# Optimization experiments

Measured on AMD Instinct MI355X. Metric: run time of the kernel, lower is better.

Reference implementation:

```python
import jax, jax.numpy as jnp
import numpy as np

ITERATIONS = 2   # init kwarg 'iterations'
EPS = 1e-7


def squash(s):
    # squash along last axis (dims_out), matching squash(..., axis=-2) on [..., dims, 1]
    sq_norm = jnp.sum(s * s, axis=-1, keepdims=True)
    return (sq_norm / (1.0 + sq_norm)) * s / jnp.sqrt(sq_norm + EPS)


def setup_inputs() -> dict:
    key = jax.random.key(0)
    kx, kw = jax.random.split(key)
    B, C_IN, D_IN = 64, 2048, 8    # batch, input capsules, input capsule dims
    K, D_OUT = 32, 16              # output capsules (caps), output dims (dims)
    x = jax.random.normal(kx, (B, C_IN, D_IN), dtype=jnp.float32)
    # W ~ Normal(0, 0.1) as in add_weight initializer; stored [K, C_IN, D_OUT, D_IN]
    W = jax.random.normal(kw, (K, C_IN, D_OUT, D_IN), dtype=jnp.float32) * 0.1
    return {"x": x, "W": W}


def reference(x, W):
    # predictions u[b,k,c,i] = sum_j W[k,c,i,j] * x[b,c,j]
    u = jnp.einsum('kcij,bcj->bkci', W, x)          # [B, K, C, D_OUT]
    B, K, C, D = u.shape
    logits = jnp.zeros((B, K, C), dtype=u.dtype)
    v = jnp.zeros((B, K, D), dtype=u.dtype)         # initial_outputs = 0
    for _ in range(ITERATIONS):
        # agreement[b,k,c] = <u[b,k,c,:], v[b,k,:]>  (predictions^T @ outputs)
        agreement = jnp.einsum('bkci,bki->bkc', u, v)
        logits = logits + agreement
        # softmax over output capsules (original axis=3 == caps_out dim)
        cc = jax.nn.softmax(logits, axis=1)          # [B, K, C]
        s = jnp.einsum('bkc,bkci->bki', cc, u)       # centroids: sum over caps_in
        v = squash(s)                                # [B, K, D]
    return v
```

## Files before the change

### kernel.cpp

```cpp
#include <hip/hip_runtime.h>

#define Bn 64
#define Cn 2048
#define Kn 32
#define In 16
#define EPSf 1e-7f

#define NOUT (Bn * Kn * In)
#define KJ   (Cn * 8)
#define KS1  64
#define KS2  32

typedef short bf8v __attribute__((ext_vector_type(8)));
typedef float f4v  __attribute__((ext_vector_type(4)));

union U16B { uint4 u; bf8v v; unsigned short h[8]; };

__device__ __forceinline__ unsigned short f2bf(float f) {
    unsigned u = __float_as_uint(f);
    u += 0x7FFF + ((u >> 16) & 1);
    return (unsigned short)(u >> 16);
}
__device__ __forceinline__ unsigned cvtpk(float lo, float hi) {
    unsigned r;
    asm("v_cvt_pk_bf16_f32 %0, %1, %2" : "=v"(r) : "v"(lo), "v"(hi));
    return r;
}
__device__ __forceinline__ float bflo(unsigned u) { return __uint_as_float(u << 16); }
__device__ __forceinline__ float bfhi(unsigned u) { return __uint_as_float(u & 0xffff0000u); }

__global__ __launch_bounds__(256) void kPrepX(const float* __restrict__ x,
                                              unsigned short* __restrict__ xb,
                                              unsigned short* __restrict__ xT2)
{
    const int g = blockIdx.x * 256 + threadIdx.x;
    const float4* s = (const float4*)(x + (size_t)g * 8);
    float4 a = s[0], b4 = s[1];
    U16B o;
    o.h[0] = f2bf(a.x);  o.h[1] = f2bf(a.y);  o.h[2] = f2bf(a.z);  o.h[3] = f2bf(a.w);
    o.h[4] = f2bf(b4.x); o.h[5] = f2bf(b4.y); o.h[6] = f2bf(b4.z); o.h[7] = f2bf(b4.w);
    ((uint4*)xb)[g] = o.u;
    const int b = g >> 11, c = g & 2047;
    *(uint2*)(xT2 + ((size_t)(c * 2 + 0) * 64 + b) * 4) = make_uint2(o.u.x, o.u.y);
    *(uint2*)(xT2 + ((size_t)(c * 2 + 1) * 64 + b) * 4) = make_uint2(o.u.z, o.u.w);
}

__global__ __launch_bounds__(256) void kGemm1(const unsigned short* __restrict__ xb,
                                              const float* __restrict__ W,
                                              float* __restrict__ part1)
{
    const int nstrip = blockIdx.x & 7;
    const int ksplit = blockIdx.x >> 3;
    const int ks0    = ksplit * 8;
    const int lane   = threadIdx.x & 63;
    const int m0     = (threadIdx.x >> 6) * 16;
    const int i      = lane & 15;
    const int cq     = lane >> 4;

    f4v acc[4] = {};
    const unsigned short* arow = xb + (size_t)(m0 + (lane & 15)) * KJ + cq * 8;

    for (int s = 0; s < 8; ++s) {
        const int ks = ks0 + s;
        U16B af;
        af.u = *(const uint4*)(arow + (size_t)ks * 32);
        const int c = ks * 4 + cq;
        #pragma unroll
        for (int t = 0; t < 4; ++t) {
            const int ko = nstrip * 4 + t;
            const float* wp = W + (((size_t)ko * Cn + c) * 16 + i) * 8;
            const float4 w0 = *(const float4*)wp;
            const float4 w1 = *(const float4*)(wp + 4);
            U16B bf;
            bf.u.x = cvtpk(w0.x, w0.y); bf.u.y = cvtpk(w0.z, w0.w);
            bf.u.z = cvtpk(w1.x, w1.y); bf.u.w = cvtpk(w1.z, w1.w);
            acc[t] = __builtin_amdgcn_mfma_f32_16x16x32_bf16(af.v, bf.v, acc[t], 0, 0, 0);
        }
    }

    float* pb = part1 + (size_t)ksplit * NOUT;
    const int col = lane & 15, rbase = (lane >> 4) * 4;
    #pragma unroll
    for (int t = 0; t < 4; ++t) {
        const int n = (nstrip * 4 + t) * 16 + col;
        #pragma unroll
        for (int r = 0; r < 4; ++r)
            pb[(size_t)(m0 + rbase + r) * 512 + n] = acc[t][r];
    }
}

__global__ __launch_bounds__(256) void kSq1(const float* __restrict__ part1,
                                            unsigned short* __restrict__ v1f)
{
    const int t = blockIdx.x * 256 + threadIdx.x;
    float s = 0.f;
    #pragma unroll 8
    for (int g = 0; g < KS1; ++g) s += part1[(size_t)g * NOUT + t];
    s *= (1.0f / 32.0f);
    float sq = s * s;
    sq += __shfl_xor(sq, 1);
    sq += __shfl_xor(sq, 2);
    sq += __shfl_xor(sq, 4);
    sq += __shfl_xor(sq, 8);
    const float f = (sq / (1.0f + sq)) * rsqrtf(sq + EPSf);
    const float v = s * f;
    const int b = t >> 9, k = (t >> 4) & 31, i = t & 15;
    const int pos = ((k * 4 + (b >> 4)) * 32 + (i >> 3) * 16 + (b & 15)) * 8 + (i & 7);
    v1f[pos] = f2bf(v);
}

__global__ __launch_bounds__(256) void kAgr(const float* __restrict__ W,
                                            const unsigned short* __restrict__ v1f,
                                            const unsigned short* __restrict__ xT2,
                                            float* __restrict__ agr)
{
    const int ko   = blockIdx.x & 31;
    const int cg   = blockIdx.x >> 5;
    const int lane = threadIdx.x & 63;
    const int w    = threadIdx.x >> 6;

    U16B bfr[4];
    #pragma unroll
    for (int nt = 0; nt < 4; ++nt) {
        if (lane < 32)
            bfr[nt].u = *(const uint4*)(v1f + ((size_t)(ko * 4 + nt) * 32 + lane) * 8);
        else
            bfr[nt].u = make_uint4(0, 0, 0, 0);
    }

    for (int mt = w; mt < 32; mt += 4) {
        const int cjb = cg * 512 + mt * 16;
        U16B afr;
        if (lane < 32) {
            const int cj = cjb + (lane & 15);
            const int c = cj >> 3, j = cj & 7;
            const int ib = (lane >> 4) * 8;
            const float* wp = W + (((size_t)ko * Cn + c) * 16 + ib) * 8 + j;
            afr.u.x = cvtpk(wp[0],  wp[8]);
            afr.u.y = cvtpk(wp[16], wp[24]);
            afr.u.z = cvtpk(wp[32], wp[40]);
            afr.u.w = cvtpk(wp[48], wp[56]);
        } else afr.u = make_uint4(0, 0, 0, 0);

        const int xrow = (cjb >> 2) + (lane >> 4);
        #pragma unroll
        for (int nt = 0; nt < 4; ++nt) {
            f4v acc = {0.f, 0.f, 0.f, 0.f};
            acc = __builtin_amdgcn_mfma_f32_16x16x32_bf16(afr.v, bfr[nt].v, acc, 0, 0, 0);
            const int b = nt * 16 + (lane & 15);
            const uint2 xq = *(const uint2*)(xT2 + ((size_t)xrow * 64 + b) * 4);
            float p = acc[0] * bflo(xq.x) + acc[1] * bfhi(xq.x)
                    + acc[2] * bflo(xq.y) + acc[3] * bfhi(xq.y);
            p += __shfl_xor(p, 16);
            if (!(lane & 16)) {
                const int c = (cjb >> 3) + (lane >> 5);
                agr[((size_t)ko * Cn + c) * 64 + b] = p;
            }
        }
    }
}

__global__ __launch_bounds__(256) void kSmax(float* __restrict__ agr)
{
    const int t = blockIdx.x * 256 + threadIdx.x;
    float* base = agr + (size_t)(t >> 6) * 64 + (t & 63);
    float a[32];
    float mx = -1e30f;
    #pragma unroll
    for (int k = 0; k < 32; ++k) { a[k] = base[(size_t)k * (Cn * 64)]; mx = fmaxf(mx, a[k]); }
    float sum = 0.f;
    #pragma unroll
    for (int k = 0; k < 32; ++k) { a[k] = __expf(a[k] - mx); sum += a[k]; }
    const float r = 1.0f / sum;
    #pragma unroll
    for (int k = 0; k < 32; ++k) base[(size_t)k * (Cn * 64)] = a[k] * r;
}

__global__ __launch_bounds__(256) void kGemm2(const unsigned short* __restrict__ xb,
                                              const float* __restrict__ W,
                                              const float* __restrict__ cc,
                                              float* __restrict__ part2)
{
    const int ko    = blockIdx.x & 31;
    const int split = blockIdx.x >> 5;
    const int ks0   = split * 16;
    const int lane  = threadIdx.x & 63;
    const int m0    = (threadIdx.x >> 6) * 16;
    const int i     = lane & 15;
    const int cq    = lane >> 4;
    const int bg    = m0 + (lane & 15);

    f4v acc = {0.f, 0.f, 0.f, 0.f};
    const unsigned short* arow = xb + (size_t)bg * KJ + cq * 8;
    const float* ccp = cc + ((size_t)ko * Cn + ks0 * 4 + cq) * 64 + bg;

    for (int s = 0; s < 16; ++s) {
        const int ks = ks0 + s;
        const int c  = ks * 4 + cq;
        const uint4 au = *(const uint4*)(arow + (size_t)ks * 32);
        const float cv = ccp[s * 256];
        U16B af;
        af.u.x = cvtpk(bflo(au.x) * cv, bfhi(au.x) * cv);
        af.u.y = cvtpk(bflo(au.y) * cv, bfhi(au.y) * cv);
        af.u.z = cvtpk(bflo(au.z) * cv, bfhi(au.z) * cv);
        af.u.w = cvtpk(bflo(au.w) * cv, bfhi(au.w) * cv);
        const float* wp = W + (((size_t)ko * Cn + c) * 16 + i) * 8;
        const float4 w0 = *(const float4*)wp;
        const float4 w1 = *(const float4*)(wp + 4);
        U16B bf;
        bf.u.x = cvtpk(w0.x, w0.y); bf.u.y = cvtpk(w0.z, w0.w);
        bf.u.z = cvtpk(w1.x, w1.y); bf.u.w = cvtpk(w1.z, w1.w);
        acc = __builtin_amdgcn_mfma_f32_16x16x32_bf16(af.v, bf.v, acc, 0, 0, 0);
    }

    float* pb = part2 + (size_t)split * NOUT;
    const int col = lane & 15, rbase = (lane >> 4) * 4;
    #pragma unroll
    for (int r = 0; r < 4; ++r)
        pb[(size_t)(m0 + rbase + r) * 512 + ko * 16 + col] = acc[r];
}

__global__ __launch_bounds__(256) void kSq2(const float* __restrict__ part2,
                                            float* __restrict__ out)
{
    const int t = blockIdx.x * 256 + threadIdx.x;
    const size_t o = (size_t)t * 4;
    float4 s = make_float4(0.f, 0.f, 0.f, 0.f);
    #pragma unroll 8
    for (int g = 0; g < KS2; ++g) {
        const float4 p = *(const float4*)(part2 + (size_t)g * NOUT + o);
        s.x += p.x; s.y += p.y; s.z += p.z; s.w += p.w;
    }
    float sq = (s.x * s.x + s.y * s.y) + (s.z * s.z + s.w * s.w);
    sq += __shfl_xor(sq, 1);
    sq += __shfl_xor(sq, 2);
    const float f = (sq / (1.0f + sq)) * rsqrtf(sq + EPSf);
    *(float4*)(out + o) = make_float4(s.x * f, s.y * f, s.z * f, s.w * f);
}

extern "C" void kernel_launch(void* const* d_in, const int* in_sizes, int n_in,
                              void* d_out, int out_size, void* d_ws, size_t ws_size,
                              hipStream_t stream)
{
    const float* x = (const float*)d_in[0];
    const float* W = (const float*)d_in[1];
    float* out = (float*)d_out;

    float* wsf = (float*)d_ws;
    float*          agr   = wsf;
    float*          part1 = wsf;
    unsigned short* xb    = (unsigned short*)(wsf + 4194304);
    unsigned short* xT2   = (unsigned short*)(wsf + 4194304 + 524288);
    float*          part2 = wsf + 4194304 + 524288;
    unsigned short* v1f   = (unsigned short*)(wsf + 4194304 + 524288 + 1048576);

    kPrepX<<<512,  256, 0, stream>>>(x, xb, xT2);
    kGemm1<<<512,  256, 0, stream>>>(xb, W, part1);
    kSq1  <<<128,  256, 0, stream>>>(part1, v1f);
    kAgr  <<<1024, 256, 0, stream>>>(W, v1f, xT2, agr);
    kSmax <<<512,  256, 0, stream>>>(agr);
    kGemm2<<<1024, 256, 0, stream>>>(xb, W, agr, part2);
    kSq2  <<<32,   256, 0, stream>>>(part2, out);
}
```

Before: 136.6 us.

## Fuse all routing stages into one cooperative persistent kernel with grid syncs

Merges the seven separate kernels into a single cooperative kernel of 512 blocks. Stages are separated by grid-wide barriers, and the code falls back to per-phase launches if the cooperative launch fails. Each stage is re-partitioned to fit the fixed 512-block grid: agreement and the second GEMM do twice the work per block, the split-K of the second GEMM drops from 32 to 16, and the reductions use shared memory. The goal is to remove launch gaps between kernels. In exchange it adds grid-sync cost, fewer blocks for the larger phases, and register pressure from the combined kernel.

Result: slower. 505.6 us (+270.2%).

```diff
diff --git a/kernel.cpp b/kernel.cpp
--- a/kernel.cpp
+++ b/kernel.cpp
@@ -1,15 +1,15 @@
 #include <hip/hip_runtime.h>
-
-#define Bn 64
+#include <hip/hip_cooperative_groups.h>
+
+namespace cg = cooperative_groups;
+
 #define Cn 2048
-#define Kn 32
-#define In 16
 #define EPSf 1e-7f
 
-#define NOUT (Bn * Kn * In)
-#define KJ   (Cn * 8)
+#define NOUT 32768
+#define KJ   16384
 #define KS1  64
-#define KS2  32
+#define KS2  16
 
 typedef short bf8v __attribute__((ext_vector_type(8)));
 typedef float f4v  __attribute__((ext_vector_type(4)));
@@ -29,213 +29,232 @@
 __device__ __forceinline__ float bflo(unsigned u) { return __uint_as_float(u << 16); }
 __device__ __forceinline__ float bfhi(unsigned u) { return __uint_as_float(u & 0xffff0000u); }
 
-__global__ __launch_bounds__(256) void kPrepX(const float* __restrict__ x,
-                                              unsigned short* __restrict__ xb,
-                                              unsigned short* __restrict__ xT2)
+__global__ __launch_bounds__(256, 4) void kFused(const float* __restrict__ x,
+                                                 const float* __restrict__ W,
+                                                 float* __restrict__ out,
+                                                 float* __restrict__ wsf,
+                                                 int phase)
 {
-    const int g = blockIdx.x * 256 + threadIdx.x;
-    const float4* s = (const float4*)(x + (size_t)g * 8);
-    float4 a = s[0], b4 = s[1];
-    U16B o;
-    o.h[0] = f2bf(a.x);  o.h[1] = f2bf(a.y);  o.h[2] = f2bf(a.z);  o.h[3] = f2bf(a.w);
-    o.h[4] = f2bf(b4.x); o.h[5] = f2bf(b4.y); o.h[6] = f2bf(b4.z); o.h[7] = f2bf(b4.w);
-    ((uint4*)xb)[g] = o.u;
-    const int b = g >> 11, c = g & 2047;
-    *(uint2*)(xT2 + ((size_t)(c * 2 + 0) * 64 + b) * 4) = make_uint2(o.u.x, o.u.y);
-    *(uint2*)(xT2 + ((size_t)(c * 2 + 1) * 64 + b) * 4) = make_uint2(o.u.z, o.u.w);
-}
-
-__global__ __launch_bounds__(256) void kGemm1(const unsigned short* __restrict__ xb,
-                                              const float* __restrict__ W,
-                                              float* __restrict__ part1)
-{
-    const int nstrip = blockIdx.x & 7;
-    const int ksplit = blockIdx.x >> 3;
-    const int ks0    = ksplit * 8;
-    const int lane   = threadIdx.x & 63;
-    const int m0     = (threadIdx.x >> 6) * 16;
-    const int i      = lane & 15;
-    const int cq     = lane >> 4;
-
-    f4v acc[4] = {};
-    const unsigned short* arow = xb + (size_t)(m0 + (lane & 15)) * KJ + cq * 8;
-
-    for (int s = 0; s < 8; ++s) {
-        const int ks = ks0 + s;
-        U16B af;
-        af.u = *(const uint4*)(arow + (size_t)ks * 32);
-        const int c = ks * 4 + cq;
+    float*          agr   = wsf;
+    float*          part1 = wsf;
+    unsigned short* xb    = (unsigned short*)(wsf + 4194304);
+    unsigned short* xT2   = (unsigned short*)(wsf + 4718592);
+    float*          part2 = wsf + 4718592;
+    unsigned short* v1f   = (unsigned short*)(wsf + 5242880);
+
+    cg::grid_group grid = cg::this_grid();
+    const int  bid  = blockIdx.x;
+    const int  tid  = threadIdx.x;
+    const int  lane = tid & 63;
+    const bool all  = (phase < 0);
+
+    __shared__ float  shA[4][65];
+    __shared__ float4 shB[256];
+
+    if (all || phase == 0) {
+        const int g = bid * 256 + tid;
+        const float4* s = (const float4*)(x + (size_t)g * 8);
+        float4 a = s[0], b4 = s[1];
+        U16B o;
+        o.h[0] = f2bf(a.x);  o.h[1] = f2bf(a.y);  o.h[2] = f2bf(a.z);  o.h[3] = f2bf(a.w);
+        o.h[4] = f2bf(b4.x); o.h[5] = f2bf(b4.y); o.h[6] = f2bf(b4.z); o.h[7] = f2bf(b4.w);
+        ((uint4*)xb)[g] = o.u;
+        const int b = g >> 11, c = g & 2047;
+        *(uint2*)(xT2 + ((size_t)(c * 2 + 0) * 64 + b) * 4) = make_uint2(o.u.x, o.u.y);
+        *(uint2*)(xT2 + ((size_t)(c * 2 + 1) * 64 + b) * 4) = make_uint2(o.u.z, o.u.w);
+    }
+    if (all) grid.sync();
+
+    if (all || phase == 1) {
+        const int nstrip = bid & 7;
+        const int ksplit = bid >> 3;
+        const int ks0    = ksplit * 8;
+        const int m0     = (tid >> 6) * 16;
+        const int i      = lane & 15;
+        const int cq     = lane >> 4;
+
+        f4v acc[4] = {};
+        const unsigned short* arow = xb + (size_t)(m0 + i) * KJ + cq * 8;
+
+        for (int s = 0; s < 8; ++s) {
+            const int ks = ks0 + s;
+            U16B af;
+            af.u = *(const uint4*)(arow + (size_t)ks * 32);
+            const int c = ks * 4 + cq;
+            #pragma unroll
+            for (int t = 0; t < 4; ++t) {
+                const int ko = nstrip * 4 + t;
+                const float* wp = W + (((size_t)ko * Cn + c) * 16 + i) * 8;
+                const float4 w0 = *(const float4*)wp;
+                const float4 w1 = *(const float4*)(wp + 4);
+                U16B bf;
+                bf.u.x = cvtpk(w0.x, w0.y); bf.u.y = cvtpk(w0.z, w0.w);
+                bf.u.z = cvtpk(w1.x, w1.y); bf.u.w = cvtpk(w1.z, w1.w);
+                acc[t] = __builtin_amdgcn_mfma_f32_16x16x32_bf16(af.v, bf.v, acc[t], 0, 0, 0);
+            }
+        }
+        float* pb = part1 + (size_t)ksplit * NOUT;
+        const int col = lane & 15, rbase = (lane >> 4) * 4;
         #pragma unroll
         for (int t = 0; t < 4; ++t) {
-            const int ko = nstrip * 4 + t;
+            const int n = (nstrip * 4 + t) * 16 + col;
+            #pragma unroll
+            for (int r = 0; r < 4; ++r)
+                pb[(size_t)(m0 + rbase + r) * 512 + n] = acc[t][r];
+        }
+    }
+    if (all) grid.sync();
+
+    if (all || phase == 2) {
+        const int itemL = tid & 63, sub = tid >> 6;
+        const int item  = bid * 64 + itemL;
+        float s = 0.f;
+        #pragma unroll 4
+        for (int g = 0; g < 16; ++g)
+            s += part1[(size_t)(sub * 16 + g) * NOUT + item];
+        shA[sub][itemL] = s;
+        __syncthreads();
+        if (tid < 64) {
+            float s2 = (shA[0][tid] + shA[1][tid]) + (shA[2][tid] + shA[3][tid]);
+            s2 *= (1.0f / 32.0f);
+            float sq = s2 * s2;
+            sq += __shfl_xor(sq, 1);
+            sq += __shfl_xor(sq, 2);
+            sq += __shfl_xor(sq, 4);
+            sq += __shfl_xor(sq, 8);
+            const float f = (sq / (1.0f + sq)) * rsqrtf(sq + EPSf);
+            const float v = s2 * f;
+            const int it = bid * 64 + tid;
+            const int b = it >> 9, k = (it >> 4) & 31, ii = it & 15;
+            const int pos = ((k * 4 + (b >> 4)) * 32 + (ii >> 3) * 16 + (b & 15)) * 8 + (ii & 7);
+            v1f[pos] = f2bf(v);
+        }
+    }
+    if (all) grid.sync();
+
+    if (all || phase == 3) {
+        const int ko  = bid & 31;
+        const int cgi = bid >> 5;
+        const int w   = tid >> 6;
+
+        U16B bfr[4];
+        #pragma unroll
+        for (int nt = 0; nt < 4; ++nt) {
+            if (lane < 32)
+                bfr[nt].u = *(const uint4*)(v1f + ((size_t)(ko * 4 + nt) * 32 + lane) * 8);
+            else
+                bfr[nt].u = make_uint4(0, 0, 0, 0);
+        }
+
+        for (int mt = w; mt < 64; mt += 4) {
+            const int cjb = cgi * 1024 + mt * 16;
+            U16B afr;
+            if (lane < 32) {
+                const int cj = cjb + (lane & 15);
+                const int c = cj >> 3, j = cj & 7;
+                const int ib = (lane >> 4) * 8;
+                const float* wp = W + (((size_t)ko * Cn + c) * 16 + ib) * 8 + j;
+                afr.u.x = cvtpk(wp[0],  wp[8]);
+                afr.u.y = cvtpk(wp[16], wp[24]);
+                afr.u.z = cvtpk(wp[32], wp[40]);
+                afr.u.w = cvtpk(wp[48], wp[56]);
+            } else afr.u = make_uint4(0, 0, 0, 0);
+
+            const int xrow = (cjb >> 2) + (lane >> 4);
+            #pragma unroll
+            for (int nt = 0; nt < 4; ++nt) {
+                f4v acc = {0.f, 0.f, 0.f, 0.f};
+                acc = __builtin_amdgcn_mfma_f32_16x16x32_bf16(afr.v, bfr[nt].v, acc, 0, 0, 0);
+                const int b = nt * 16 + (lane & 15);
+                const uint2 xq = *(const uint2*)(xT2 + ((size_t)xrow * 64 + b) * 4);
+                float p = acc[0] * bflo(xq.x) + acc[1] * bfhi(xq.x)
+                        + acc[2] * bflo(xq.y) + acc[3] * bfhi(xq.y);
+                p += __shfl_xor(p, 16);
+                if (!(lane & 16)) {
+                    const int c = (cjb >> 3) + (lane >> 5);
+                    agr[((size_t)ko * Cn + c) * 64 + b] = p;
+                }
+            }
+        }
+    }
+    if (all) grid.sync();
+
+    if (all || phase == 4) {
+        const int t = bid * 256 + tid;
+        float* base = agr + (size_t)(t >> 6) * 64 + (t & 63);
+        float a[32];
+        float mx = -1e30f;
+        #pragma unroll
+        for (int k = 0; k < 32; ++k) { a[k] = base[(size_t)k * (Cn * 64)]; mx = fmaxf(mx, a[k]); }
+        float sum = 0.f;
+        #pragma unroll
+        for (int k = 0; k < 32; ++k) { a[k] = __expf(a[k] - mx); sum += a[k]; }
+        const float r = 1.0f / sum;
+        #pragma unroll
+        for (int k = 0; k < 32; ++k) base[(size_t)k * (Cn * 64)] = a[k] * r;
+    }
+    if (all) grid.sync();
+
+    if (all || phase == 5) {
+        const int ko    = bid & 31;
+        const int split = bid >> 5;
+        const int ks0   = split * 32;
+        const int m0    = (tid >> 6) * 16;
+        const int i     = lane & 15;
+        const int cq    = lane >> 4;
+        const int bg    = m0 + i;
+
+        f4v acc = {0.f, 0.f, 0.f, 0.f};
+        const unsigned short* arow = xb + (size_t)bg * KJ + cq * 8;
+        const float* ccp = agr + ((size_t)ko * Cn + ks0 * 4 + cq) * 64 + bg;
+
+        for (int s = 0; s < 32; ++s) {
+            const int ks = ks0 + s;
+            const int c  = ks * 4 + cq;
+            const uint4 au = *(const uint4*)(arow + (size_t)ks * 32);
+            const float cv = ccp[s * 256];
+            U16B af;
+            af.u.x = cvtpk(bflo(au.x) * cv, bfhi(au.x) * cv);
+            af.u.y = cvtpk(bflo(au.y) * cv, bfhi(au.y) * cv);
+            af.u.z = cvtpk(bflo(au.z) * cv, bfhi(au.z) * cv);
+            af.u.w = cvtpk(bflo(au.w) * cv, bfhi(au.w) * cv);
             const float* wp = W + (((size_t)ko * Cn + c) * 16 + i) * 8;
             const float4 w0 = *(const float4*)wp;
             const float4 w1 = *(const float4*)(wp + 4);
             U16B bf;
             bf.u.x = cvtpk(w0.x, w0.y); bf.u.y = cvtpk(w0.z, w0.w);
             bf.u.z = cvtpk(w1.x, w1.y); bf.u.w = cvtpk(w1.z, w1.w);
-            acc[t] = __builtin_amdgcn_mfma_f32_16x16x32_bf16(af.v, bf.v, acc[t], 0, 0, 0);
-        }
-    }
-
-    float* pb = part1 + (size_t)ksplit * NOUT;
-    const int col = lane & 15, rbase = (lane >> 4) * 4;
-    #pragma unroll
-    for (int t = 0; t < 4; ++t) {
-        const int n = (nstrip * 4 + t) * 16 + col;
+            acc = __builtin_amdgcn_mfma_f32_16x16x32_bf16(af.v, bf.v, acc, 0, 0, 0);
+        }
+
+        float* pb = part2 + (size_t)split * NOUT;
+        const int col = lane & 15, rbase = (lane >> 4) * 4;
         #pragma unroll
         for (int r = 0; r < 4; ++r)
-            pb[(size_t)(m0 + rbase + r) * 512 + n] = acc[t][r];
-    }
-}
-
-__global__ __launch_bounds__(256) void kSq1(const float* __restrict__ part1,
-                                            unsigned short* __restrict__ v1f)
-{
-    const int t = blockIdx.x * 256 + threadIdx.x;
-    float s = 0.f;
-    #pragma unroll 8
-    for (int g = 0; g < KS1; ++g) s += part1[(size_t)g * NOUT + t];
-    s *= (1.0f / 32.0f);
-    float sq = s * s;
-    sq += __shfl_xor(sq, 1);
-    sq += __shfl_xor(sq, 2);
-    sq += __shfl_xor(sq, 4);
-    sq += __shfl_xor(sq, 8);
-    const float f = (sq / (1.0f + sq)) * rsqrtf(sq + EPSf);
-    const float v = s * f;
-    const int b = t >> 9, k = (t >> 4) & 31, i = t & 15;
-    const int pos = ((k * 4 + (b >> 4)) * 32 + (i >> 3) * 16 + (b & 15)) * 8 + (i & 7);
-    v1f[pos] = f2bf(v);
-}
-
-__global__ __launch_bounds__(256) void kAgr(const float* __restrict__ W,
-                                            const unsigned short* __restrict__ v1f,
-                                            const unsigned short* __restrict__ xT2,
-                                            float* __restrict__ agr)
-{
-    const int ko   = blockIdx.x & 31;
-    const int cg   = blockIdx.x >> 5;
-    const int lane = threadIdx.x & 63;
-    const int w    = threadIdx.x >> 6;
-
-    U16B bfr[4];
-    #pragma unroll
-    for (int nt = 0; nt < 4; ++nt) {
-        if (lane < 32)
-            bfr[nt].u = *(const uint4*)(v1f + ((size_t)(ko * 4 + nt) * 32 + lane) * 8);
-        else
-            bfr[nt].u = make_uint4(0, 0, 0, 0);
-    }
-
-    for (int mt = w; mt < 32; mt += 4) {
-        const int cjb = cg * 512 + mt * 16;
-        U16B afr;
-        if (lane < 32) {
-            const int cj = cjb + (lane & 15);
-            const int c = cj >> 3, j = cj & 7;
-            const int ib = (lane >> 4) * 8;
-            const float* wp = W + (((size_t)ko * Cn + c) * 16 + ib) * 8 + j;
-            afr.u.x = cvtpk(wp[0],  wp[8]);
-            afr.u.y = cvtpk(wp[16], wp[24]);
-            afr.u.z = cvtpk(wp[32], wp[40]);
-            afr.u.w = cvtpk(wp[48], wp[56]);
-        } else afr.u = make_uint4(0, 0, 0, 0);
-
-        const int xrow = (cjb >> 2) + (lane >> 4);
-        #pragma unroll
-        for (int nt = 0; nt < 4; ++nt) {
-            f4v acc = {0.f, 0.f, 0.f, 0.f};
-            acc = __builtin_amdgcn_mfma_f32_16x16x32_bf16(afr.v, bfr[nt].v, acc, 0, 0, 0);
-            const int b = nt * 16 + (lane & 15);
-            const uint2 xq = *(const uint2*)(xT2 + ((size_t)xrow * 64 + b) * 4);
-            float p = acc[0] * bflo(xq.x) + acc[1] * bfhi(xq.x)
-                    + acc[2] * bflo(xq.y) + acc[3] * bfhi(xq.y);
-            p += __shfl_xor(p, 16);
-            if (!(lane & 16)) {
-                const int c = (cjb >> 3) + (lane >> 5);
-                agr[((size_t)ko * Cn + c) * 64 + b] = p;
+            pb[(size_t)(m0 + rbase + r) * 512 + ko * 16 + col] = acc[r];
+    }
+    if (all) grid.sync();
+
+    if (all || phase == 6) {
+        const int itemL = tid & 15, sub = tid >> 4;
+        const int item  = bid * 16 + itemL;
+        shB[tid] = *(const float4*)(part2 + (size_t)sub * NOUT + (size_t)item * 4);
+        __syncthreads();
+        if (tid < 16) {
+            float4 s = make_float4(0.f, 0.f, 0.f, 0.f);
+            #pragma unroll
+            for (int sb = 0; sb < 16; ++sb) {
+                const float4 q = shB[sb * 16 + tid];
+                s.x += q.x; s.y += q.y; s.z += q.z; s.w += q.w;
             }
-        }
-    }
-}
-
-__global__ __launch_bounds__(256) void kSmax(float* __restrict__ agr)
-{
-    const int t = blockIdx.x * 256 + threadIdx.x;
-    float* base = agr + (size_t)(t >> 6) * 64 + (t & 63);
-    float a[32];
-    float mx = -1e30f;
-    #pragma unroll
-    for (int k = 0; k < 32; ++k) { a[k] = base[(size_t)k * (Cn * 64)]; mx = fmaxf(mx, a[k]); }
-    float sum = 0.f;
-    #pragma unroll
-    for (int k = 0; k < 32; ++k) { a[k] = __expf(a[k] - mx); sum += a[k]; }
-    const float r = 1.0f / sum;
-    #pragma unroll
-    for (int k = 0; k < 32; ++k) base[(size_t)k * (Cn * 64)] = a[k] * r;
-}
-
-__global__ __launch_bounds__(256) void kGemm2(const unsigned short* __restrict__ xb,
-                                              const float* __restrict__ W,
-                                              const float* __restrict__ cc,
-                                              float* __restrict__ part2)
-{
-    const int ko    = blockIdx.x & 31;
-    const int split = blockIdx.x >> 5;
-    const int ks0   = split * 16;
-    const int lane  = threadIdx.x & 63;
-    const int m0    = (threadIdx.x >> 6) * 16;
-    const int i     = lane & 15;
-    const int cq    = lane >> 4;
-    const int bg    = m0 + (lane & 15);
-
-    f4v acc = {0.f, 0.f, 0.f, 0.f};
-    const unsigned short* arow = xb + (size_t)bg * KJ + cq * 8;
-    const float* ccp = cc + ((size_t)ko * Cn + ks0 * 4 + cq) * 64 + bg;
-
-    for (int s = 0; s < 16; ++s) {
-        const int ks = ks0 + s;
-        const int c  = ks * 4 + cq;
-        const uint4 au = *(const uint4*)(arow + (size_t)ks * 32);
-        const float cv = ccp[s * 256];
-        U16B af;
-        af.u.x = cvtpk(bflo(au.x) * cv, bfhi(au.x) * cv);
-        af.u.y = cvtpk(bflo(au.y) * cv, bfhi(au.y) * cv);
-        af.u.z = cvtpk(bflo(au.z) * cv, bfhi(au.z) * cv);
-        af.u.w = cvtpk(bflo(au.w) * cv, bfhi(au.w) * cv);
-        const float* wp = W + (((size_t)ko * Cn + c) * 16 + i) * 8;
-        const float4 w0 = *(const float4*)wp;
-        const float4 w1 = *(const float4*)(wp + 4);
-        U16B bf;
-        bf.u.x = cvtpk(w0.x, w0.y); bf.u.y = cvtpk(w0.z, w0.w);
-        bf.u.z = cvtpk(w1.x, w1.y); bf.u.w = cvtpk(w1.z, w1.w);
-        acc = __builtin_amdgcn_mfma_f32_16x16x32_bf16(af.v, bf.v, acc, 0, 0, 0);
-    }
-
-    float* pb = part2 + (size_t)split * NOUT;
-    const int col = lane & 15, rbase = (lane >> 4) * 4;
-    #pragma unroll
-    for (int r = 0; r < 4; ++r)
-        pb[(size_t)(m0 + rbase + r) * 512 + ko * 16 + col] = acc[r];
-}
-
-__global__ __launch_bounds__(256) void kSq2(const float* __restrict__ part2,
-                                            float* __restrict__ out)
-{
-    const int t = blockIdx.x * 256 + threadIdx.x;
-    const size_t o = (size_t)t * 4;
-    float4 s = make_float4(0.f, 0.f, 0.f, 0.f);
-    #pragma unroll 8
-    for (int g = 0; g < KS2; ++g) {
-        const float4 p = *(const float4*)(part2 + (size_t)g * NOUT + o);
-        s.x += p.x; s.y += p.y; s.z += p.z; s.w += p.w;
-    }
-    float sq = (s.x * s.x + s.y * s.y) + (s.z * s.z + s.w * s.w);
-    sq += __shfl_xor(sq, 1);
-    sq += __shfl_xor(sq, 2);
-    const float f = (sq / (1.0f + sq)) * rsqrtf(sq + EPSf);
-    *(float4*)(out + o) = make_float4(s.x * f, s.y * f, s.z * f, s.w * f);
+            float sq = (s.x * s.x + s.y * s.y) + (s.z * s.z + s.w * s.w);
+            sq += __shfl_xor(sq, 1);
+            sq += __shfl_xor(sq, 2);
+            const float f = (sq / (1.0f + sq)) * rsqrtf(sq + EPSf);
+            *(float4*)(out + (size_t)(bid * 16 + tid) * 4) =
+                make_float4(s.x * f, s.y * f, s.z * f, s.w * f);
+        }
+    }
 }
 
 extern "C" void kernel_launch(void* const* d_in, const int* in_sizes, int n_in,
@@ -245,20 +264,16 @@
     const float* x = (const float*)d_in[0];
     const float* W = (const float*)d_in[1];
     float* out = (float*)d_out;
-
     float* wsf = (float*)d_ws;
-    float*          agr   = wsf;
-    float*          part1 = wsf;
-    unsigned short* xb    = (unsigned short*)(wsf + 4194304);
-    unsigned short* xT2   = (unsigned short*)(wsf + 4194304 + 524288);
-    float*          part2 = wsf + 4194304 + 524288;
-    unsigned short* v1f   = (unsigned short*)(wsf + 4194304 + 524288 + 1048576);
-
-    kPrepX<<<512,  256, 0, stream>>>(x, xb, xT2);
-    kGemm1<<<512,  256, 0, stream>>>(xb, W, part1);
-    kSq1  <<<128,  256, 0, stream>>>(part1, v1f);
-    kAgr  <<<1024, 256, 0, stream>>>(W, v1f, xT2, agr);
-    kSmax <<<512,  256, 0, stream>>>(agr);
-    kGemm2<<<1024, 256, 0, stream>>>(xb, W, agr, part2);
-    kSq2  <<<32,   256, 0, stream>>>(part2, out);
-}
+
+    int phase = -1;
+    void* args[] = { (void*)&x, (void*)&W, (void*)&out, (void*)&wsf, (void*)&phase };
+    hipError_t err = hipLaunchCooperativeKernel((const void*)kFused, dim3(512),
+                                                dim3(256), args, 0, stream);
+    if (err != hipSuccess) {
+        (void)hipGetLastError();
+        for (int p = 0; p < 7; ++p)
+            hipLaunchKernelGGL(kFused, dim3(512), dim3(256), 0, stream,
+                               x, W, out, wsf, p);
+    }
+}
```
